# Performance work log

Hardware: AMD Instinct MI355X
Metric: run time of the kernel (lower is better)

Reference implementation:

```python
import jax, jax.numpy as jnp
import numpy as np

B, N, D, F_IN, F_OUT, MAX_DEG = 256, 512, 6, 128, 128, 6


def setup_inputs() -> dict:
    key = jax.random.key(0)
    k_atoms, k_deg, k_idx, k_w, k_b = jax.random.split(key, 5)
    atoms = jax.random.normal(k_atoms, (B, N, F_IN), dtype=jnp.float32)
    # structured edges: per-atom degree in [0, MAX_DEG-1], valid neighbor ids in
    # the first `deg` slots, -1 padding afterwards (NGFP convention)
    deg = jax.random.randint(k_deg, (B, N, 1), 0, MAX_DEG)
    nbr = jax.random.randint(k_idx, (B, N, D), 0, N)
    slot = jnp.arange(D)[None, None, :]
    edges = jnp.where(slot < deg, nbr, -1).astype(jnp.int64)
    W = jax.random.normal(k_w, (MAX_DEG, F_IN, F_OUT), dtype=jnp.float32) * (1.0 / np.sqrt(F_IN))
    b = jax.random.normal(k_b, (MAX_DEG, F_OUT), dtype=jnp.float32) * 0.01
    return {"atoms": atoms, "edges": edges, "W": W, "b": b}


def reference(atoms, edges, W, b):
    # lookup_neighbors with include_self=True: gather neighbor rows (-1 -> zero row)
    atoms_p = jnp.pad(atoms, ((0, 0), (1, 0), (0, 0)))          # [B, N+1, F]; row 0 is zeros
    gathered = jax.vmap(lambda a, e: a[e])(atoms_p, edges + 1)  # [B, N, D, F]
    summed = gathered.sum(axis=-2) + atoms                      # [B, N, F] (self included)
    degrees = (edges != -1).sum(axis=-1, keepdims=True)         # [B, N, 1]
    out = jnp.zeros(summed.shape[:-1] + (W.shape[-1],), dtype=summed.dtype)
    for d in range(MAX_DEG):
        h = jax.nn.relu(summed @ W[d] + b[d])                   # [B, N, F_OUT]
        out = out + h * (degrees == d).astype(summed.dtype)
    return out
```

## Files before the change

### kernel.cpp

```cpp
#include <hip/hip_runtime.h>


typedef short bf16x8 __attribute__((ext_vector_type(8)));
typedef float f32x4  __attribute__((ext_vector_type(4)));
typedef unsigned short ushort_t;
typedef unsigned int uint_t;

constexpr int Nn = 512;
constexpr int Ff = 128;
constexpr int BN = 256 * 512;
constexpr int NB = BN / 256;

constexpr size_t WS_DEG    = 0;
constexpr size_t WS_CNT    = 131072;
constexpr size_t WS_OFFS   = 143360;
constexpr size_t WS_DBASE  = 155648;
constexpr size_t WS_SORTED = 155680;
constexpr size_t WS_WT     = 679968;
constexpr size_t WS_NEEDED = 876576;

__device__ inline ushort_t f2bf(float f) {
    uint_t u = __float_as_uint(f);
    return (ushort_t)((u + 0x7FFFu + ((u >> 16) & 1u)) >> 16);
}

__device__ inline bool detect_is64(const int* edges32) {
    int probe = edges32[2 * (threadIdx.x & 63) + 1];
    return __any(probe > 0) == 0;
}

__global__ __launch_bounds__(256)
void k0_deg(const int* __restrict__ edges32, unsigned char* __restrict__ degw,
            int* __restrict__ cnt) {
    const int tid = threadIdx.x, b = blockIdx.x;
    const int a = b * 256 + tid;
    const bool is64 = detect_is64(edges32);
    int dg = 0;
    #pragma unroll
    for (int j = 0; j < 6; j++) {
        int e = is64 ? edges32[((size_t)a * 6 + j) * 2] : edges32[(size_t)a * 6 + j];
        dg += (e != -1) ? 1 : 0;
    }
    degw[a] = (unsigned char)dg;
    __shared__ int h[6];
    if (tid < 6) h[tid] = 0;
    __syncthreads();
    atomicAdd(&h[dg], 1);
    __syncthreads();
    if (tid < 6) cnt[tid * NB + b] = h[tid];
}

__global__ __launch_bounds__(512)
void k1_scan(const int* __restrict__ cnt, int* __restrict__ offs,
             int* __restrict__ deg_base) {
    const int t = threadIdx.x;
    const int lane = t & 63, w = t >> 6;
    __shared__ int wsum[8], wpre[8];
    __shared__ int baseSh, totSh;
    if (t == 0) baseSh = 0;
    __syncthreads();
    for (int d = 0; d < 6; d++) {
        const int baseLocal = baseSh;
        const int v = cnt[d * NB + t];
        int incl = v;
        #pragma unroll
        for (int s = 1; s < 64; s <<= 1) {
            int o = __shfl_up(incl, (unsigned)s, 64);
            if (lane >= s) incl += o;
        }
        if (lane == 63) wsum[w] = incl;
        __syncthreads();
        if (t == 0) {
            int acc = 0;
            for (int i = 0; i < 8; i++) { wpre[i] = acc; acc += wsum[i]; }
            totSh = acc;
        }
        __syncthreads();
        offs[d * NB + t] = baseLocal + wpre[w] + (incl - v);
        if (t == 0) { deg_base[d] = baseLocal; baseSh = baseLocal + totSh; }
        __syncthreads();
    }
    if (t == 0) deg_base[6] = baseSh;
}

__global__ __launch_bounds__(256)
void k2_scatter(const unsigned char* __restrict__ degw, const int* __restrict__ offs,
                int* __restrict__ sorted) {
    const int tid = threadIdx.x, b = blockIdx.x;
    const int a = b * 256 + tid;
    __shared__ unsigned char degs[256];
    const int dg = degw[a];
    degs[tid] = (unsigned char)dg;
    __syncthreads();
    int rank = 0;
    for (int j = 0; j < tid; j++) rank += (degs[j] == dg) ? 1 : 0;
    sorted[offs[dg * NB + b] + rank] = a;
}

__global__ __launch_bounds__(256)
void kw_conv(const float* __restrict__ W, ushort_t* __restrict__ Wt) {
    const int idx = blockIdx.x * 256 + threadIdx.x;
    const int d = idx >> 14, r = idx & 16383;
    const int k = r >> 7, n = r & 127;
    Wt[d * 16384 + n * 128 + k] = f2bf(W[idx]);
}

__global__ __launch_bounds__(256, 2)
void k3_gemm(const float* __restrict__ atoms,
             const int* __restrict__ edges32,
             const float* __restrict__ bias,
             const ushort_t* __restrict__ Wt,
             const int* __restrict__ sorted,
             const int* __restrict__ deg_base,
             float* __restrict__ out) {
    const int d = blockIdx.x;
    const int t = blockIdx.y;
    const int base = deg_base[d];
    const int total = deg_base[d + 1] - base;
    const int m0 = t * 128;
    if (m0 >= total) return;
    const int nrows = min(128, total - m0);

    __shared__ __attribute__((aligned(16))) ushort_t Ash[128 * 136];
    __shared__ __attribute__((aligned(16))) ushort_t Bsh[128 * 136];
    __shared__ int ids_sh[128];

    const int tid = threadIdx.x;
    const bool is64 = detect_is64(edges32);

    if (tid < 128) {
        int idx = m0 + tid;
        if (idx >= total) idx = total - 1;
        ids_sh[tid] = sorted[base + idx];
    }
    __syncthreads();

    {
        const uint4* Wg = (const uint4*)(Wt + (size_t)d * 16384);
        #pragma unroll
        for (int i = 0; i < 8; i++) {
            int idx = tid + i * 256;
            int n = idx >> 4, c = idx & 15;
            uint4 v = Wg[idx];
            *(uint4*)&Bsh[n * 136 + c * 8] = v;
        }
    }

    {
        const int r = tid >> 1, h = tid & 1;
        const int aId = ids_sh[r];
        const int mol = aId & ~(Nn - 1);
        const float4* self4 = (const float4*)(atoms + (size_t)aId * Ff + h * 64);
        float4 acc[16];
        #pragma unroll
        for (int c = 0; c < 16; c++) acc[c] = self4[c];
        #pragma unroll
        for (int j = 0; j < 6; j++) {
            int e = is64 ? edges32[((size_t)aId * 6 + j) * 2]
                         : edges32[(size_t)aId * 6 + j];
            if (e >= 0) {
                const float4* nb4 = (const float4*)(atoms + (size_t)(mol + e) * Ff + h * 64);
                #pragma unroll
                for (int c = 0; c < 16; c++) {
                    float4 v = nb4[c];
                    acc[c].x += v.x; acc[c].y += v.y; acc[c].z += v.z; acc[c].w += v.w;
                }
            }
        }
        ushort_t* dst = &Ash[r * 136 + h * 64];
        #pragma unroll
        for (int c8 = 0; c8 < 8; c8++) {
            float4 p = acc[2 * c8], q = acc[2 * c8 + 1];
            uint4 o;
            o.x = (uint_t)f2bf(p.x) | ((uint_t)f2bf(p.y) << 16);
            o.y = (uint_t)f2bf(p.z) | ((uint_t)f2bf(p.w) << 16);
            o.z = (uint_t)f2bf(q.x) | ((uint_t)f2bf(q.y) << 16);
            o.w = (uint_t)f2bf(q.z) | ((uint_t)f2bf(q.w) << 16);
            *(uint4*)(dst + c8 * 8) = o;
        }
    }
    __syncthreads();

    {
        const int lane = tid & 63, w = tid >> 6;
        const int mrow = w * 32;
        const int kq = lane >> 4;
        const int ml = lane & 15;

        bf16x8 af[2][4];
        #pragma unroll
        for (int mt = 0; mt < 2; mt++)
            #pragma unroll
            for (int k0 = 0; k0 < 4; k0++)
                af[mt][k0] = *(const bf16x8*)&Ash[(mrow + mt * 16 + ml) * 136 + k0 * 32 + kq * 8];

        #pragma unroll
        for (int nt = 0; nt < 8; nt++) {
            bf16x8 bfr[4];
            #pragma unroll
            for (int k0 = 0; k0 < 4; k0++)
                bfr[k0] = *(const bf16x8*)&Bsh[(nt * 16 + ml) * 136 + k0 * 32 + kq * 8];
            f32x4 c0 = {0.f, 0.f, 0.f, 0.f}, c1 = {0.f, 0.f, 0.f, 0.f};
            #pragma unroll
            for (int k0 = 0; k0 < 4; k0++) {
                c0 = __builtin_amdgcn_mfma_f32_16x16x32_bf16(af[0][k0], bfr[k0], c0, 0, 0, 0);
                c1 = __builtin_amdgcn_mfma_f32_16x16x32_bf16(af[1][k0], bfr[k0], c1, 0, 0, 0);
            }
            const int col = nt * 16 + ml;
            const float bcol = bias[d * Ff + col];
            #pragma unroll
            for (int mt = 0; mt < 2; mt++) {
                f32x4 cc = mt ? c1 : c0;
                #pragma unroll
                for (int reg = 0; reg < 4; reg++) {
                    int r = mrow + mt * 16 + kq * 4 + reg;
                    if (r < nrows) {
                        float v = cc[reg] + bcol;
                        out[(size_t)ids_sh[r] * Ff + col] = v > 0.f ? v : 0.f;
                    }
                }
            }
        }
    }
}

__global__ __launch_bounds__(128, 2)
void graphconv_fallback(const float* __restrict__ atoms,
                        const int* __restrict__ edges_raw,
                        const float* __restrict__ W,
                        const float* __restrict__ bias,
                        float* __restrict__ out) {
    const int tid = threadIdx.x;
    const int d = blockIdx.x % 6;
    const int k = blockIdx.x / 6;
    const int a0 = k * 256;
    __shared__ int eds[256 * 6];
    __shared__ int list[256];
    __shared__ int cnt;
    __shared__ float sv[2][Ff];
    bool is64;
    { int v = edges_raw[2 * (tid & 63) + 1]; is64 = (__ballot(v > 0) == 0ull); }
    if (!is64) { for (int i = tid; i < 256 * 6; i += 128) eds[i] = edges_raw[a0 * 6 + i]; }
    else       { for (int i = tid; i < 256 * 6; i += 128) eds[i] = edges_raw[2 * (a0 * 6 + i)]; }
    if (tid == 0) cnt = 0;
    __syncthreads();
    for (int i = tid; i < 256; i += 128) {
        int deg = 0;
        #pragma unroll
        for (int j = 0; j < 6; j++) deg += (eds[i * 6 + j] != -1) ? 1 : 0;
        if (deg == d) { int p = atomicAdd(&cnt, 1); list[p] = i; }
    }
    float Wreg[Ff];
    { const float* Wd = W + (size_t)d * Ff * Ff;
      #pragma unroll
      for (int f = 0; f < Ff; f++) Wreg[f] = Wd[f * Ff + tid]; }
    const float breg = bias[d * Ff + tid];
    __syncthreads();
    const int n = cnt;
    const float* batch_atoms = atoms + (size_t)(a0 / Nn) * Nn * Ff;
    const int row0 = a0 % Nn;
    for (int ii = 0; ii < n; ii++) {
        const int i = list[ii];
        float s = batch_atoms[(row0 + i) * Ff + tid];
        #pragma unroll
        for (int j = 0; j < 6; j++) {
            int e = eds[i * 6 + j];
            if (e != -1) s += batch_atoms[e * Ff + tid];
        }
        float* buf = sv[ii & 1];
        buf[tid] = s;
        __syncthreads();
        float acc = breg;
        const float4* sv4 = (const float4*)buf;
        #pragma unroll
        for (int fc = 0; fc < Ff / 4; fc++) {
            float4 x = sv4[fc];
            acc = fmaf(x.x, Wreg[4 * fc + 0], acc);
            acc = fmaf(x.y, Wreg[4 * fc + 1], acc);
            acc = fmaf(x.z, Wreg[4 * fc + 2], acc);
            acc = fmaf(x.w, Wreg[4 * fc + 3], acc);
        }
        out[(size_t)(a0 + i) * Ff + tid] = fmaxf(acc, 0.0f);
    }
}

extern "C" void kernel_launch(void* const* d_in, const int* in_sizes, int n_in,
                              void* d_out, int out_size, void* d_ws, size_t ws_size,
                              hipStream_t stream) {
    const float* atoms = (const float*)d_in[0];
    const int*   edges = (const int*)d_in[1];
    const float* W     = (const float*)d_in[2];
    const float* bias  = (const float*)d_in[3];
    float*       outp  = (float*)d_out;

    if (ws_size >= WS_NEEDED) {
        char* ws = (char*)d_ws;
        unsigned char* degw = (unsigned char*)(ws + WS_DEG);
        int* cnt    = (int*)(ws + WS_CNT);
        int* offs   = (int*)(ws + WS_OFFS);
        int* dbase  = (int*)(ws + WS_DBASE);
        int* sorted = (int*)(ws + WS_SORTED);
        ushort_t* Wt = (ushort_t*)(ws + WS_WT);

        k0_deg<<<NB, 256, 0, stream>>>(edges, degw, cnt);
        kw_conv<<<384, 256, 0, stream>>>(W, Wt);
        k1_scan<<<1, 512, 0, stream>>>(cnt, offs, dbase);
        k2_scatter<<<NB, 256, 0, stream>>>(degw, offs, sorted);
        k3_gemm<<<dim3(6, 1024), 256, 0, stream>>>(atoms, edges, bias, Wt, sorted, dbase, outp);
    } else {
        graphconv_fallback<<<3072, 128, 0, stream>>>(atoms, edges, W, bias, outp);
    }
}
```

Measured before the change: 189.0 us.

## Fuse degree bucketing, weight conversion and neighbor sum into one pre-pass

Replaces the degree count, scan, scatter and weight-conversion kernels with one pre-pass. It buckets atoms by degree using wave ballots plus global atomic counters, converts W to transposed bf16, and writes the neighbor-summed activations as bf16 to a workspace buffer. The GEMM kernel then reads those rows directly into registers instead of gathering and summing neighbors itself, which cuts its shared memory and allows higher occupancy. The cost is an extra round trip of a 32 MB bf16 intermediate through memory and a larger workspace requirement. If the workspace is too small, the fallback kernel runs instead.

```diff
diff --git a/kernel.cpp b/kernel.cpp
--- a/kernel.cpp
+++ b/kernel.cpp
@@ -9,15 +9,12 @@
 constexpr int Nn = 512;
 constexpr int Ff = 128;
 constexpr int BN = 256 * 512;
-constexpr int NB = BN / 256;
-
-constexpr size_t WS_DEG    = 0;
-constexpr size_t WS_CNT    = 131072;
-constexpr size_t WS_OFFS   = 143360;
-constexpr size_t WS_DBASE  = 155648;
-constexpr size_t WS_SORTED = 155680;
-constexpr size_t WS_WT     = 679968;
-constexpr size_t WS_NEEDED = 876576;
+
+constexpr size_t WS_GC     = 0;
+constexpr size_t WS_REGION = 256;
+constexpr size_t WS_WT     = 256 + (size_t)6 * BN * 4;
+constexpr size_t WS_SUMMED = WS_WT + 196608;
+constexpr size_t WS_NEEDED = WS_SUMMED + (size_t)BN * 128 * 2;
 
 __device__ inline ushort_t f2bf(float f) {
     uint_t u = __float_as_uint(f);
@@ -29,195 +26,164 @@
     return __any(probe > 0) == 0;
 }
 
-__global__ __launch_bounds__(256)
-void k0_deg(const int* __restrict__ edges32, unsigned char* __restrict__ degw,
-            int* __restrict__ cnt) {
-    const int tid = threadIdx.x, b = blockIdx.x;
-    const int a = b * 256 + tid;
+__global__ __launch_bounds__(256, 3)
+void k1_pre(const float* __restrict__ atoms,
+            const int*   __restrict__ edges32,
+            const float* __restrict__ W,
+            int* __restrict__ gcnt,
+            int* __restrict__ region,
+            ushort_t* __restrict__ Wt,
+            ushort_t* __restrict__ summed) {
+    const int tid = threadIdx.x;
+    const int blk = blockIdx.x;
+    const int c0  = blk * 128;
     const bool is64 = detect_is64(edges32);
-    int dg = 0;
+
+    __shared__ int eds_sh[128 * 6];
+    __shared__ int wcnt[2][6];
+    __shared__ int base_sh[6];
+
+    if (blk < 96) {
+        #pragma unroll
+        for (int i = 0; i < 4; i++) {
+            int linear = blk * 1024 + i * 256 + tid;
+            int d = linear >> 14, rem = linear & 16383;
+            int k = rem >> 7, n = rem & 127;
+            Wt[d * 16384 + n * 128 + k] = f2bf(W[linear]);
+        }
+    }
+
+    int dg = 0, rank = 0;
+    if (tid < 128) {
+        const int a = c0 + tid;
+        #pragma unroll
+        for (int j = 0; j < 6; j++) {
+            int e = is64 ? edges32[((size_t)a * 6 + j) * 2]
+                         : edges32[(size_t)a * 6 + j];
+            eds_sh[tid * 6 + j] = e;
+            dg += (e != -1) ? 1 : 0;
+        }
+        const int lane = tid & 63, w = tid >> 6;
+        unsigned long long bal[6];
+        #pragma unroll
+        for (int dv = 0; dv < 6; dv++) bal[dv] = __ballot(dg == dv);
+        if (lane < 6) wcnt[w][lane] = (int)__popcll(bal[lane]);
+        unsigned long long below = (lane == 0) ? 0ull : (bal[dg] << (64 - lane));
+        rank = (int)__popcll(bal[dg] & ((lane == 63) ? 0x7FFFFFFFFFFFFFFFull
+                                                     : ((1ull << lane) - 1ull)));
+        (void)below;
+    }
+    __syncthreads();
+    if (tid < 6) base_sh[tid] = atomicAdd(&gcnt[tid], wcnt[0][tid] + wcnt[1][tid]);
+    __syncthreads();
+    if (tid < 128) {
+        int pos = base_sh[dg] + ((tid >> 6) ? wcnt[0][dg] : 0) + rank;
+        region[dg * BN + pos] = c0 + tid;
+    }
+
+    const int r = tid >> 1, h = tid & 1;
+    const int a = c0 + r;
+    const int molbase = c0 & ~(Nn - 1);
+    const float4* self4 = (const float4*)(atoms + (size_t)a * Ff + h * 64);
+    float4 acc[16];
+    #pragma unroll
+    for (int c = 0; c < 16; c++) acc[c] = self4[c];
     #pragma unroll
     for (int j = 0; j < 6; j++) {
-        int e = is64 ? edges32[((size_t)a * 6 + j) * 2] : edges32[(size_t)a * 6 + j];
-        dg += (e != -1) ? 1 : 0;
-    }
-    degw[a] = (unsigned char)dg;
-    __shared__ int h[6];
-    if (tid < 6) h[tid] = 0;
-    __syncthreads();
-    atomicAdd(&h[dg], 1);
-    __syncthreads();
-    if (tid < 6) cnt[tid * NB + b] = h[tid];
-}
-
-__global__ __launch_bounds__(512)
-void k1_scan(const int* __restrict__ cnt, int* __restrict__ offs,
-             int* __restrict__ deg_base) {
-    const int t = threadIdx.x;
-    const int lane = t & 63, w = t >> 6;
-    __shared__ int wsum[8], wpre[8];
-    __shared__ int baseSh, totSh;
-    if (t == 0) baseSh = 0;
-    __syncthreads();
-    for (int d = 0; d < 6; d++) {
-        const int baseLocal = baseSh;
-        const int v = cnt[d * NB + t];
-        int incl = v;
-        #pragma unroll
-        for (int s = 1; s < 64; s <<= 1) {
-            int o = __shfl_up(incl, (unsigned)s, 64);
-            if (lane >= s) incl += o;
-        }
-        if (lane == 63) wsum[w] = incl;
-        __syncthreads();
-        if (t == 0) {
-            int acc = 0;
-            for (int i = 0; i < 8; i++) { wpre[i] = acc; acc += wsum[i]; }
-            totSh = acc;
-        }
-        __syncthreads();
-        offs[d * NB + t] = baseLocal + wpre[w] + (incl - v);
-        if (t == 0) { deg_base[d] = baseLocal; baseSh = baseLocal + totSh; }
-        __syncthreads();
-    }
-    if (t == 0) deg_base[6] = baseSh;
-}
-
-__global__ __launch_bounds__(256)
-void k2_scatter(const unsigned char* __restrict__ degw, const int* __restrict__ offs,
-                int* __restrict__ sorted) {
-    const int tid = threadIdx.x, b = blockIdx.x;
-    const int a = b * 256 + tid;
-    __shared__ unsigned char degs[256];
-    const int dg = degw[a];
-    degs[tid] = (unsigned char)dg;
-    __syncthreads();
-    int rank = 0;
-    for (int j = 0; j < tid; j++) rank += (degs[j] == dg) ? 1 : 0;
-    sorted[offs[dg * NB + b] + rank] = a;
-}
-
-__global__ __launch_bounds__(256)
-void kw_conv(const float* __restrict__ W, ushort_t* __restrict__ Wt) {
-    const int idx = blockIdx.x * 256 + threadIdx.x;
-    const int d = idx >> 14, r = idx & 16383;
-    const int k = r >> 7, n = r & 127;
-    Wt[d * 16384 + n * 128 + k] = f2bf(W[idx]);
-}
-
-__global__ __launch_bounds__(256, 2)
-void k3_gemm(const float* __restrict__ atoms,
-             const int* __restrict__ edges32,
-             const float* __restrict__ bias,
+        int e = eds_sh[r * 6 + j];
+        if (e >= 0) {
+            const float4* nb4 = (const float4*)(atoms + (size_t)(molbase + e) * Ff + h * 64);
+            #pragma unroll
+            for (int c = 0; c < 16; c++) {
+                float4 v = nb4[c];
+                acc[c].x += v.x; acc[c].y += v.y; acc[c].z += v.z; acc[c].w += v.w;
+            }
+        }
+    }
+    uint4* dst = (uint4*)(summed + (size_t)a * Ff + h * 64);
+    #pragma unroll
+    for (int c8 = 0; c8 < 8; c8++) {
+        float4 p = acc[2 * c8], q = acc[2 * c8 + 1];
+        uint4 o;
+        o.x = (uint_t)f2bf(p.x) | ((uint_t)f2bf(p.y) << 16);
+        o.y = (uint_t)f2bf(p.z) | ((uint_t)f2bf(p.w) << 16);
+        o.z = (uint_t)f2bf(q.x) | ((uint_t)f2bf(q.y) << 16);
+        o.w = (uint_t)f2bf(q.z) | ((uint_t)f2bf(q.w) << 16);
+        dst[c8] = o;
+    }
+}
+
+__global__ __launch_bounds__(256, 4)
+void k2_gemm(const ushort_t* __restrict__ summed,
+             const float*    __restrict__ bias,
              const ushort_t* __restrict__ Wt,
-             const int* __restrict__ sorted,
-             const int* __restrict__ deg_base,
-             float* __restrict__ out) {
+             const int*      __restrict__ region,
+             const int*      __restrict__ gcnt,
+             float*          __restrict__ out) {
     const int d = blockIdx.x;
     const int t = blockIdx.y;
-    const int base = deg_base[d];
-    const int total = deg_base[d + 1] - base;
+    const int count = gcnt[d];
     const int m0 = t * 128;
-    if (m0 >= total) return;
-    const int nrows = min(128, total - m0);
-
-    __shared__ __attribute__((aligned(16))) ushort_t Ash[128 * 136];
+    if (m0 >= count) return;
+    const int nrows = min(128, count - m0);
+
     __shared__ __attribute__((aligned(16))) ushort_t Bsh[128 * 136];
-    __shared__ int ids_sh[128];
+    __shared__ int ids[128];
 
     const int tid = threadIdx.x;
-    const bool is64 = detect_is64(edges32);
-
     if (tid < 128) {
         int idx = m0 + tid;
-        if (idx >= total) idx = total - 1;
-        ids_sh[tid] = sorted[base + idx];
-    }
-    __syncthreads();
-
+        if (idx >= count) idx = count - 1;
+        ids[tid] = region[d * BN + idx];
+    }
     {
         const uint4* Wg = (const uint4*)(Wt + (size_t)d * 16384);
         #pragma unroll
         for (int i = 0; i < 8; i++) {
             int idx = tid + i * 256;
             int n = idx >> 4, c = idx & 15;
-            uint4 v = Wg[idx];
-            *(uint4*)&Bsh[n * 136 + c * 8] = v;
-        }
-    }
-
-    {
-        const int r = tid >> 1, h = tid & 1;
-        const int aId = ids_sh[r];
-        const int mol = aId & ~(Nn - 1);
-        const float4* self4 = (const float4*)(atoms + (size_t)aId * Ff + h * 64);
-        float4 acc[16];
-        #pragma unroll
-        for (int c = 0; c < 16; c++) acc[c] = self4[c];
-        #pragma unroll
-        for (int j = 0; j < 6; j++) {
-            int e = is64 ? edges32[((size_t)aId * 6 + j) * 2]
-                         : edges32[(size_t)aId * 6 + j];
-            if (e >= 0) {
-                const float4* nb4 = (const float4*)(atoms + (size_t)(mol + e) * Ff + h * 64);
-                #pragma unroll
-                for (int c = 0; c < 16; c++) {
-                    float4 v = nb4[c];
-                    acc[c].x += v.x; acc[c].y += v.y; acc[c].z += v.z; acc[c].w += v.w;
-                }
-            }
-        }
-        ushort_t* dst = &Ash[r * 136 + h * 64];
-        #pragma unroll
-        for (int c8 = 0; c8 < 8; c8++) {
-            float4 p = acc[2 * c8], q = acc[2 * c8 + 1];
-            uint4 o;
-            o.x = (uint_t)f2bf(p.x) | ((uint_t)f2bf(p.y) << 16);
-            o.y = (uint_t)f2bf(p.z) | ((uint_t)f2bf(p.w) << 16);
-            o.z = (uint_t)f2bf(q.x) | ((uint_t)f2bf(q.y) << 16);
-            o.w = (uint_t)f2bf(q.z) | ((uint_t)f2bf(q.w) << 16);
-            *(uint4*)(dst + c8 * 8) = o;
-        }
-    }
-    __syncthreads();
-
-    {
-        const int lane = tid & 63, w = tid >> 6;
-        const int mrow = w * 32;
-        const int kq = lane >> 4;
-        const int ml = lane & 15;
-
-        bf16x8 af[2][4];
-        #pragma unroll
-        for (int mt = 0; mt < 2; mt++)
+            *(uint4*)&Bsh[n * 136 + c * 8] = Wg[idx];
+        }
+    }
+    __syncthreads();
+
+    const int lane = tid & 63, w = tid >> 6;
+    const int mrow = w * 32;
+    const int kq = lane >> 4;
+    const int ml = lane & 15;
+
+    bf16x8 af[2][4];
+    #pragma unroll
+    for (int mt = 0; mt < 2; mt++) {
+        const int row = ids[mrow + mt * 16 + ml];
+        const bf16x8* sp = (const bf16x8*)(summed + (size_t)row * Ff + kq * 8);
+        #pragma unroll
+        for (int k0 = 0; k0 < 4; k0++) af[mt][k0] = sp[k0 * 4];
+    }
+
+    #pragma unroll
+    for (int nt = 0; nt < 8; nt++) {
+        bf16x8 bfr[4];
+        #pragma unroll
+        for (int k0 = 0; k0 < 4; k0++)
+            bfr[k0] = *(const bf16x8*)&Bsh[(nt * 16 + ml) * 136 + k0 * 32 + kq * 8];
+        f32x4 c0 = {0.f, 0.f, 0.f, 0.f}, c1 = {0.f, 0.f, 0.f, 0.f};
+        #pragma unroll
+        for (int k0 = 0; k0 < 4; k0++) {
+            c0 = __builtin_amdgcn_mfma_f32_16x16x32_bf16(af[0][k0], bfr[k0], c0, 0, 0, 0);
+            c1 = __builtin_amdgcn_mfma_f32_16x16x32_bf16(af[1][k0], bfr[k0], c1, 0, 0, 0);
+        }
+        const int col = nt * 16 + ml;
+        const float bcol = bias[d * Ff + col];
+        #pragma unroll
+        for (int mt = 0; mt < 2; mt++) {
+            f32x4 cc = mt ? c1 : c0;
             #pragma unroll
-            for (int k0 = 0; k0 < 4; k0++)
-                af[mt][k0] = *(const bf16x8*)&Ash[(mrow + mt * 16 + ml) * 136 + k0 * 32 + kq * 8];
-
-        #pragma unroll
-        for (int nt = 0; nt < 8; nt++) {
-            bf16x8 bfr[4];
-            #pragma unroll
-            for (int k0 = 0; k0 < 4; k0++)
-                bfr[k0] = *(const bf16x8*)&Bsh[(nt * 16 + ml) * 136 + k0 * 32 + kq * 8];
-            f32x4 c0 = {0.f, 0.f, 0.f, 0.f}, c1 = {0.f, 0.f, 0.f, 0.f};
-            #pragma unroll
-            for (int k0 = 0; k0 < 4; k0++) {
-                c0 = __builtin_amdgcn_mfma_f32_16x16x32_bf16(af[0][k0], bfr[k0], c0, 0, 0, 0);
-                c1 = __builtin_amdgcn_mfma_f32_16x16x32_bf16(af[1][k0], bfr[k0], c1, 0, 0, 0);
-            }
-            const int col = nt * 16 + ml;
-            const float bcol = bias[d * Ff + col];
-            #pragma unroll
-            for (int mt = 0; mt < 2; mt++) {
-                f32x4 cc = mt ? c1 : c0;
-                #pragma unroll
-                for (int reg = 0; reg < 4; reg++) {
-                    int r = mrow + mt * 16 + kq * 4 + reg;
-                    if (r < nrows) {
-                        float v = cc[reg] + bcol;
-                        out[(size_t)ids_sh[r] * Ff + col] = v > 0.f ? v : 0.f;
-                    }
+            for (int reg = 0; reg < 4; reg++) {
+                int rl = mrow + mt * 16 + kq * 4 + reg;
+                if (rl < nrows) {
+                    float v = cc[reg] + bcol;
+                    out[(size_t)ids[rl] * Ff + col] = v > 0.f ? v : 0.f;
                 }
             }
         }
@@ -295,18 +261,14 @@
 
     if (ws_size >= WS_NEEDED) {
         char* ws = (char*)d_ws;
-        unsigned char* degw = (unsigned char*)(ws + WS_DEG);
-        int* cnt    = (int*)(ws + WS_CNT);
-        int* offs   = (int*)(ws + WS_OFFS);
-        int* dbase  = (int*)(ws + WS_DBASE);
-        int* sorted = (int*)(ws + WS_SORTED);
-        ushort_t* Wt = (ushort_t*)(ws + WS_WT);
-
-        k0_deg<<<NB, 256, 0, stream>>>(edges, degw, cnt);
-        kw_conv<<<384, 256, 0, stream>>>(W, Wt);
-        k1_scan<<<1, 512, 0, stream>>>(cnt, offs, dbase);
-        k2_scatter<<<NB, 256, 0, stream>>>(degw, offs, sorted);
-        k3_gemm<<<dim3(6, 1024), 256, 0, stream>>>(atoms, edges, bias, Wt, sorted, dbase, outp);
+        int*      gcnt   = (int*)(ws + WS_GC);
+        int*      region = (int*)(ws + WS_REGION);
+        ushort_t* Wt     = (ushort_t*)(ws + WS_WT);
+        ushort_t* summed = (ushort_t*)(ws + WS_SUMMED);
+
+        hipMemsetAsync(gcnt, 0, 32, stream);
+        k1_pre<<<1024, 256, 0, stream>>>(atoms, edges, W, gcnt, region, Wt, summed);
+        k2_gemm<<<dim3(6, 1024), 256, 0, stream>>>(summed, bias, Wt, region, gcnt, outp);
     } else {
         graphconv_fallback<<<3072, 128, 0, stream>>>(atoms, edges, W, bias, outp);
     }
```

Measured after the change: 196.5 us. 4.0% more time.
